# Kernel tuning notes

Measured on AMD Instinct MI355X. Metric: run time of the kernel, lower is better.

Reference implementation:

```python
import jax, jax.numpy as jnp
import numpy as np

T, B, I, H = 1200, 32, 512, 512


def setup_inputs() -> dict:
    key = jax.random.key(0)
    ks = jax.random.split(key, 10)
    s = 0.1
    x = jax.random.normal(ks[0], (T, B, I), dtype=jnp.float32)
    lengths = jax.random.randint(ks[1], (B,), 1, T + 1)
    lengths = lengths.at[0].set(T)  # ensure padded output length == T (static shape)
    return {
        "x": x,
        "output_lengths": lengths,
        "w_ih_fwd": jax.random.normal(ks[2], (4 * H, I), dtype=jnp.float32) * s,
        "w_hh_fwd": jax.random.normal(ks[3], (4 * H, H), dtype=jnp.float32) * s,
        "b_ih_fwd": jax.random.normal(ks[4], (4 * H,), dtype=jnp.float32) * s,
        "b_hh_fwd": jax.random.normal(ks[5], (4 * H,), dtype=jnp.float32) * s,
        "w_ih_bwd": jax.random.normal(ks[6], (4 * H, I), dtype=jnp.float32) * s,
        "w_hh_bwd": jax.random.normal(ks[7], (4 * H, H), dtype=jnp.float32) * s,
        "b_ih_bwd": jax.random.normal(ks[8], (4 * H,), dtype=jnp.float32) * s,
        "b_hh_bwd": jax.random.normal(ks[9], (4 * H,), dtype=jnp.float32) * s,
    }


def _lstm_dir(x, mask, w_ih, w_hh, b_ih, b_hh):
    """Masked unidirectional LSTM (PyTorch gate order i,f,g,o).
    x: (T,B,I), mask: (T,B,1) bool. Returns outputs (T,B,H), (h_n, c_n)."""
    h0 = jnp.zeros((x.shape[1], w_hh.shape[1]), dtype=x.dtype)
    c0 = jnp.zeros_like(h0)
    # Precompute input projection for all timesteps at once (one big GEMM).
    x_proj = jnp.einsum('tbi,gi->tbg', x, w_ih) + (b_ih + b_hh)

    def step(carry, inp):
        h, c = carry
        xp, m = inp  # xp: (B,4H), m: (B,1)
        gates = xp + h @ w_hh.T
        i, f, g, o = jnp.split(gates, 4, axis=-1)
        i = jax.nn.sigmoid(i)
        f = jax.nn.sigmoid(f)
        g = jnp.tanh(g)
        o = jax.nn.sigmoid(o)
        c_new = f * c + i * g
        h_new = o * jnp.tanh(c_new)
        # Packed semantics: state frozen past each sequence's length.
        h = jnp.where(m, h_new, h)
        c = jnp.where(m, c_new, c)
        out = jnp.where(m, h_new, jnp.zeros_like(h_new))  # pad positions -> 0
        return (h, c), out

    (h_n, c_n), outs = jax.lax.scan(step, (h0, c0), (x_proj, mask))
    return outs, h_n, c_n


def reference(x, output_lengths, w_ih_fwd, w_hh_fwd, b_ih_fwd, b_hh_fwd,
              w_ih_bwd, w_hh_bwd, b_ih_bwd, b_hh_bwd):
    t_idx = jnp.arange(x.shape[0])  # (T,)
    mask = (t_idx[:, None] < output_lengths[None, :])[:, :, None]  # (T,B,1)

    # Forward direction.
    out_f, h_f, c_f = _lstm_dir(x, mask, w_ih_fwd, w_hh_fwd, b_ih_fwd, b_hh_fwd)

    # Backward direction: reverse each sequence within its valid region.
    rev_idx = jnp.clip(output_lengths[None, :] - 1 - t_idx[:, None], 0)  # (T,B)
    x_rev = jnp.take_along_axis(x, rev_idx[:, :, None], axis=0) * mask
    out_r, h_b, c_b = _lstm_dir(x_rev, mask, w_ih_bwd, w_hh_bwd, b_ih_bwd, b_hh_bwd)
    out_b = jnp.take_along_axis(out_r, rev_idx[:, :, None], axis=0) * mask

    # Bidirectional view(...,2,-1).sum(2) == sum of direction outputs.
    out = out_f + out_b
    h_n = jnp.stack([h_f, h_b], axis=0)  # (2,B,H)
    c_n = jnp.stack([c_f, c_b], axis=0)
    return out, h_n, c_n
```

## Files before the change

kernel.cpp:

```cpp
#include <hip/hip_runtime.h>
#include <cstdint>
#include <cstddef>

typedef unsigned short u16;
typedef unsigned int u32;
typedef unsigned long long u64;
typedef short bf16x8 __attribute__((ext_vector_type(8)));
typedef float f32x4 __attribute__((ext_vector_type(4)));
typedef unsigned short u16x4 __attribute__((ext_vector_type(4)));

#define T_LEN 1200

#define O_X     0ull
#define O_WIH   39321600ull
#define O_WHH   43515904ull
#define O_BIAS  47710208ull
#define O_HBUF  47726592ull
#define WS_NEED 47988736ull

#define HO 19660800ull
#define CO 19693568ull

#define HROW 516

__device__ __forceinline__ u16 f2bf(float f) {
  union { float f; unsigned u; } v; v.f = f;
  unsigned r = v.u + 0x7FFFu + ((v.u >> 16) & 1u);
  return (u16)(r >> 16);
}
__device__ __forceinline__ float sigm(float x) { return 1.f / (1.f + __expf(-x)); }
__device__ __forceinline__ float tanh_s(float x) {
  float ax = fabsf(x);
  float e = __expf(-2.f * ax);
  float t = (1.f - e) / (1.f + e);
  return x < 0.f ? -t : t;
}

__device__ __forceinline__ u64 ld_dev64(const u32* p) {
  return __hip_atomic_load((const u64*)p, __ATOMIC_RELAXED, __HIP_MEMORY_SCOPE_AGENT);
}
__device__ __forceinline__ void st_dev32(u32* p, unsigned v) {
  __hip_atomic_store(p, v, __ATOMIC_RELAXED, __HIP_MEMORY_SCOPE_AGENT);
}

__global__ __launch_bounds__(256) void cast_x_k(const float4* __restrict__ x,
                                                u16* __restrict__ xb) {
  int i = blockIdx.x * 256 + threadIdx.x;
  float4 v = x[i];
  u16x4 o;
  o.x = f2bf(v.x); o.y = f2bf(v.y); o.z = f2bf(v.z); o.w = f2bf(v.w);
  *(u16x4*)(xb + (size_t)i * 4) = o;
}

__global__ __launch_bounds__(256) void prep_w_k(
    const float* __restrict__ wih_f, const float* __restrict__ whh_f,
    const float* __restrict__ bih_f, const float* __restrict__ bhh_f,
    const float* __restrict__ wih_b, const float* __restrict__ whh_b,
    const float* __restrict__ bih_b, const float* __restrict__ bhh_b,
    u16* __restrict__ Wih, u16* __restrict__ Whh, float* __restrict__ bias) {
  int tid = blockIdx.x * 256 + threadIdx.x;
  int g = tid >> 9;
  float vi, vh;
  if (g < 2048) { vi = wih_f[tid]; vh = whh_f[tid]; }
  else { int t2 = tid - (2048 * 512); vi = wih_b[t2]; vh = whh_b[t2]; }
  Wih[tid] = f2bf(vi);
  Whh[tid] = f2bf(vh);
  if ((tid & 511) == 0) {
    bias[g] = (g < 2048) ? (bih_f[g] + bhh_f[g]) : (bih_b[g - 2048] + bhh_b[g - 2048]);
  }
}

__global__ __launch_bounds__(256, 1) void lstm_rec(const u16* __restrict__ X,
                                                   const u16* __restrict__ Wih,
                                                   const u16* __restrict__ Whh,
                                                   const float* __restrict__ bias,
                                                   const int* __restrict__ lengths,
                                                   u32* __restrict__ hbuf,
                                                   float* __restrict__ out) {
  const int tid = threadIdx.x, lane = tid & 63, wid = tid >> 6;
  const int bx = blockIdx.x;
  const int dir = bx >> 5, slice = bx & 31, c0 = slice * 16;
  const int quad = lane >> 4, l15 = lane & 15;

  __shared__ alignas(16) u16 h_l[32 * HROW];
  __shared__ float pre[4][32][16];
  __shared__ int len_s[32];

  if (tid < 32) len_s[tid] = lengths[tid];

  bf16x8 bh[16], bxw[16];
  {
    const size_t wrow = (size_t)(dir * 2048 + wid * 512 + c0 + l15) * 512 + quad * 8;
#pragma unroll
    for (int ks = 0; ks < 16; ++ks) {
      bh[ks]  = *(const bf16x8*)(Whh + wrow + (size_t)ks * 32);
      bxw[ks] = *(const bf16x8*)(Wih + wrow + (size_t)ks * 32);
    }
  }
  __syncthreads();

  const int b0 = tid >> 4, colv = tid & 15, b1 = b0 + 16;
  const int hcol = c0 + colv;
  const float bi  = bias[dir * 2048 + 0 * 512 + hcol];
  const float bfv = bias[dir * 2048 + 1 * 512 + hcol];
  const float bg  = bias[dir * 2048 + 2 * 512 + hcol];
  const float bo  = bias[dir * 2048 + 3 * 512 + hcol];

  float hreg0 = 0.f, hreg1 = 0.f, creg0 = 0.f, creg1 = 0.f;
  const int len0 = len_s[b0], len1 = len_s[b1];
  const int lena = len_s[l15], lenb = len_s[16 + l15];

  for (int t = 0; t < T_LEN; ++t) {
    u32* cur = hbuf + (size_t)(((t & 1) * 2 + dir) * 16384);
    u32* nxt = hbuf + (size_t)((((t + 1) & 1) * 2 + dir) * 16384);

    int tta = (dir == 0) ? t : (lena - 1 - t);  if (tta < 0) tta = 0;
    int ttb = (dir == 0) ? t : (lenb - 1 - t);  if (ttb < 0) ttb = 0;
    const u16* xrow0 = X + ((size_t)tta * 32 + l15) * 512 + quad * 8;
    const u16* xrow1 = X + ((size_t)ttb * 32 + 16 + l15) * 512 + quad * 8;
    bf16x8 ax0[16], ax1[16];
#pragma unroll
    for (int ks = 0; ks < 16; ++ks) {
      ax0[ks] = *(const bf16x8*)(xrow0 + (size_t)ks * 32);
      ax1[ks] = *(const bf16x8*)(xrow1 + (size_t)ks * 32);
    }

    u64 stg[32];
#pragma unroll
    for (int j = 0; j < 32; ++j)
      stg[j] = ld_dev64(cur + j * 512 + tid * 2);

    f32x4 a0 = {0.f,0.f,0.f,0.f}, a1 = {0.f,0.f,0.f,0.f};
#pragma unroll
    for (int ks = 0; ks < 16; ++ks) {
      a0 = __builtin_amdgcn_mfma_f32_16x16x32_bf16(ax0[ks], bxw[ks], a0, 0, 0, 0);
      a1 = __builtin_amdgcn_mfma_f32_16x16x32_bf16(ax1[ks], bxw[ks], a1, 0, 0, 0);
    }

    const u64 e2 = ((u64)(u32)t << 32) | (u32)t;
    for (;;) {
      u64 bad = 0;
#pragma unroll
      for (int j = 0; j < 32; ++j) bad |= (stg[j] ^ e2);
      if ((bad & 0x0000FFFF0000FFFFull) == 0) break;
#pragma unroll
      for (int j = 0; j < 32; ++j)
        stg[j] = ld_dev64(cur + j * 512 + tid * 2);
    }

#pragma unroll
    for (int j = 0; j < 32; ++j) {
      u32 d0 = (u32)stg[j], d1 = (u32)(stg[j] >> 32);
      *(u32*)&h_l[j * HROW + tid * 2] = (d0 >> 16) | (d1 & 0xFFFF0000u);
    }
    __syncthreads();

    const u16* hl0 = h_l + (size_t)l15 * HROW + quad * 8;
    const u16* hl1 = h_l + (size_t)(16 + l15) * HROW + quad * 8;
#pragma unroll
    for (int ks = 0; ks < 16; ++ks) {
      bf16x8 f0 = *(const bf16x8*)(hl0 + ks * 32);
      bf16x8 f1 = *(const bf16x8*)(hl1 + ks * 32);
      a0 = __builtin_amdgcn_mfma_f32_16x16x32_bf16(f0, bh[ks], a0, 0, 0, 0);
      a1 = __builtin_amdgcn_mfma_f32_16x16x32_bf16(f1, bh[ks], a1, 0, 0, 0);
    }
#pragma unroll
    for (int r = 0; r < 4; ++r) {
      pre[wid][quad * 4 + r][l15]      = a0[r];
      pre[wid][16 + quad * 4 + r][l15] = a1[r];
    }
    __syncthreads();

    int tt0 = (dir == 0) ? t : (len0 - 1 - t);
    int tt1 = (dir == 0) ? t : (len1 - 1 - t);
    bool m0 = (dir == 0) ? (t < len0) : (tt0 >= 0);
    bool m1 = (dir == 0) ? (t < len1) : (tt1 >= 0);
    if (tt0 < 0) tt0 = 0;
    if (tt1 < 0) tt1 = 0;

    float hn0 = 0.f, hn1 = 0.f;
    if (m0) {
      float gi = pre[0][b0][colv] + bi,  gf = pre[1][b0][colv] + bfv;
      float gg = pre[2][b0][colv] + bg,  go = pre[3][b0][colv] + bo;
      float cn = sigm(gf) * creg0 + sigm(gi) * tanh_s(gg);
      hn0 = sigm(go) * tanh_s(cn);
      creg0 = cn; hreg0 = hn0;
    }
    if (m1) {
      float gi = pre[0][b1][colv] + bi,  gf = pre[1][b1][colv] + bfv;
      float gg = pre[2][b1][colv] + bg,  go = pre[3][b1][colv] + bo;
      float cn = sigm(gf) * creg1 + sigm(gi) * tanh_s(gg);
      hn1 = sigm(go) * tanh_s(cn);
      creg1 = cn; hreg1 = hn1;
    }

    const u32 tag = (u32)(t + 1);
    st_dev32(nxt + (size_t)b0 * 512 + hcol, ((u32)f2bf(hreg0) << 16) | tag);
    st_dev32(nxt + (size_t)b1 * 512 + hcol, ((u32)f2bf(hreg1) << 16) | tag);

    if (m0) atomicAdd(out + (size_t)(tt0 * 32 + b0) * 512 + hcol, hn0);
    if (m1) atomicAdd(out + (size_t)(tt1 * 32 + b1) * 512 + hcol, hn1);
  }

  out[HO + (size_t)dir * 16384 + (size_t)b0 * 512 + hcol] = hreg0;
  out[HO + (size_t)dir * 16384 + (size_t)b1 * 512 + hcol] = hreg1;
  out[CO + (size_t)dir * 16384 + (size_t)b0 * 512 + hcol] = creg0;
  out[CO + (size_t)dir * 16384 + (size_t)b1 * 512 + hcol] = creg1;
}

extern "C" void kernel_launch(void* const* d_in, const int* in_sizes, int n_in,
                              void* d_out, int out_size, void* d_ws, size_t ws_size,
                              hipStream_t stream) {
  const float* x     = (const float*)d_in[0];
  const int*   lens  = (const int*)d_in[1];
  const float* wih_f = (const float*)d_in[2];
  const float* whh_f = (const float*)d_in[3];
  const float* bih_f = (const float*)d_in[4];
  const float* bhh_f = (const float*)d_in[5];
  const float* wih_b = (const float*)d_in[6];
  const float* whh_b = (const float*)d_in[7];
  const float* bih_b = (const float*)d_in[8];
  const float* bhh_b = (const float*)d_in[9];
  float* out = (float*)d_out;
  char* ws = (char*)d_ws;

  u16*   xb   = (u16*)(ws + O_X);
  u16*   Wih  = (u16*)(ws + O_WIH);
  u16*   Whh  = (u16*)(ws + O_WHH);
  float* bias = (float*)(ws + O_BIAS);
  u32*   hbuf = (u32*)(ws + O_HBUF);

  hipMemsetAsync(hbuf, 0, 262144, stream);
  hipMemsetAsync(d_out, 0, (size_t)out_size * 4, stream);

  cast_x_k<<<19200, 256, 0, stream>>>((const float4*)x, xb);
  prep_w_k<<<8192, 256, 0, stream>>>(wih_f, whh_f, bih_f, bhh_f,
                                     wih_b, whh_b, bih_b, bhh_b, Wih, Whh, bias);
  lstm_rec<<<64, 256, 0, stream>>>(xb, Wih, Whh, bias, lens, hbuf, out);
}
```

Before: 11.26 ms.

## Co-locate each LSTM direction on one XCC and keep others busy spinning

The kernel now launches 256 blocks and uses the hardware XCC id to assign all 32 slices of a direction to the same XCC, so the per-step h exchange stays within one L2. It replaces the agent-scope atomic loads and stores with plain accesses plus an explicit cache invalidate on retry. Blocks on a third XCC run a dummy FMA spin loop, apparently to hold clocks up, and the rest exit. The x input tile is staged through LDS with split accumulators, and output atomicAdds are batched every 8 steps. This relies on undocumented XCC placement and on cache-coherence assumptions that may not hold for cross-XCC writes, and the spinning blocks burn power.

Measured after the change: 16.58 ms. +47.2%, slower.

```diff
diff --git a/kernel.cpp b/kernel.cpp
--- a/kernel.cpp
+++ b/kernel.cpp
@@ -16,7 +16,8 @@
 #define O_WHH   43515904ull
 #define O_BIAS  47710208ull
 #define O_HBUF  47726592ull
-#define WS_NEED 47988736ull
+#define O_CTL   47988736ull
+#define WS_NEED 47989248ull
 
 #define HO 19660800ull
 #define CO 19693568ull
@@ -34,13 +35,6 @@
   float e = __expf(-2.f * ax);
   float t = (1.f - e) / (1.f + e);
   return x < 0.f ? -t : t;
-}
-
-__device__ __forceinline__ u64 ld_dev64(const u32* p) {
-  return __hip_atomic_load((const u64*)p, __ATOMIC_RELAXED, __HIP_MEMORY_SCOPE_AGENT);
-}
-__device__ __forceinline__ void st_dev32(u32* p, unsigned v) {
-  __hip_atomic_store(p, v, __ATOMIC_RELAXED, __HIP_MEMORY_SCOPE_AGENT);
 }
 
 __global__ __launch_bounds__(256) void cast_x_k(const float4* __restrict__ x,
@@ -76,15 +70,70 @@
                                                    const float* __restrict__ bias,
                                                    const int* __restrict__ lengths,
                                                    u32* __restrict__ hbuf,
-                                                   float* __restrict__ out) {
+                                                   float* __restrict__ out,
+                                                   int* __restrict__ ctl) {
   const int tid = threadIdx.x, lane = tid & 63, wid = tid >> 6;
-  const int bx = blockIdx.x;
-  const int dir = bx >> 5, slice = bx & 31, c0 = slice * 16;
   const int quad = lane >> 4, l15 = lane & 15;
 
   __shared__ alignas(16) u16 h_l[32 * HROW];
+  __shared__ alignas(16) u16 x_l[32 * HROW];
   __shared__ float pre[4][32][16];
+  __shared__ float s_out[8 * 512];
   __shared__ int len_s[32];
+  __shared__ int s_dir, s_slice, s_done;
+
+  if (tid == 0) {
+    int xcc;
+    asm volatile("s_getreg_b32 %0, hwreg(HW_REG_XCC_ID)" : "=s"(xcc));
+    xcc &= 7;
+    int slot = __hip_atomic_fetch_add(&ctl[xcc], 1, __ATOMIC_RELAXED,
+                                      __HIP_MEMORY_SCOPE_AGENT);
+    int mydir;
+    if (slot == 0) {
+      int d = __hip_atomic_fetch_add(&ctl[16], 1, __ATOMIC_RELAXED,
+                                     __HIP_MEMORY_SCOPE_AGENT);
+      mydir = (d < 2) ? d : 2;
+      __hip_atomic_store(&ctl[8 + xcc], mydir + 1, __ATOMIC_RELAXED,
+                         __HIP_MEMORY_SCOPE_AGENT);
+    } else if (slot < 32) {
+      int v;
+      do {
+        v = __hip_atomic_load(&ctl[8 + xcc], __ATOMIC_RELAXED,
+                              __HIP_MEMORY_SCOPE_AGENT);
+        if (v == 0) __builtin_amdgcn_s_sleep(2);
+      } while (v == 0);
+      mydir = v - 1;
+    } else {
+      mydir = 3;
+    }
+    s_dir = mydir;
+    s_slice = (slot < 32) ? slot : 0;
+    s_done = 0;
+  }
+  __syncthreads();
+
+  if (s_dir == 3) return;
+  if (s_dir == 2) {
+    float a0 = tid * 0.5f + 1.f, a1 = tid * 0.25f + 2.f;
+    float a2 = tid * 0.125f + 3.f, a3 = tid * 0.0625f + 4.f;
+    for (;;) {
+#pragma unroll 64
+      for (int i = 0; i < 512; ++i) {
+        a0 = __builtin_fmaf(a0, 0.9999999f, 1e-9f);
+        a1 = __builtin_fmaf(a1, 0.9999998f, 2e-9f);
+        a2 = __builtin_fmaf(a2, 0.9999997f, 3e-9f);
+        a3 = __builtin_fmaf(a3, 0.9999996f, 4e-9f);
+      }
+      if (tid == 0)
+        *(volatile int*)&s_done = __hip_atomic_load(&ctl[17], __ATOMIC_RELAXED,
+                                                    __HIP_MEMORY_SCOPE_AGENT);
+      if (*(volatile int*)&s_done) break;
+    }
+    if (a0 + a1 + a2 + a3 == 3.14159f) out[0] = a0;
+    return;
+  }
+
+  const int dir = s_dir, slice = s_slice, c0 = slice * 16;
 
   if (tid < 32) len_s[tid] = lengths[tid];
 
@@ -108,34 +157,28 @@
 
   float hreg0 = 0.f, hreg1 = 0.f, creg0 = 0.f, creg1 = 0.f;
   const int len0 = len_s[b0], len1 = len_s[b1];
-  const int lena = len_s[l15], lenb = len_s[16 + l15];
+  const int xr = tid >> 3, seg = tid & 7;
+  const int lenxr = len_s[xr];
 
   for (int t = 0; t < T_LEN; ++t) {
     u32* cur = hbuf + (size_t)(((t & 1) * 2 + dir) * 16384);
     u32* nxt = hbuf + (size_t)((((t + 1) & 1) * 2 + dir) * 16384);
 
-    int tta = (dir == 0) ? t : (lena - 1 - t);  if (tta < 0) tta = 0;
-    int ttb = (dir == 0) ? t : (lenb - 1 - t);  if (ttb < 0) ttb = 0;
-    const u16* xrow0 = X + ((size_t)tta * 32 + l15) * 512 + quad * 8;
-    const u16* xrow1 = X + ((size_t)ttb * 32 + 16 + l15) * 512 + quad * 8;
-    bf16x8 ax0[16], ax1[16];
-#pragma unroll
-    for (int ks = 0; ks < 16; ++ks) {
-      ax0[ks] = *(const bf16x8*)(xrow0 + (size_t)ks * 32);
-      ax1[ks] = *(const bf16x8*)(xrow1 + (size_t)ks * 32);
-    }
+    int ttx = (dir == 0) ? t : (lenxr - 1 - t);  if (ttx < 0) ttx = 0;
+    const u16* xg = X + ((size_t)ttx * 32 + xr) * 512;
+    bf16x8 xv[8];
+#pragma unroll
+    for (int k = 0; k < 8; ++k)
+      xv[k] = *(const bf16x8*)(xg + k * 64 + seg * 8);
 
     u64 stg[32];
 #pragma unroll
     for (int j = 0; j < 32; ++j)
-      stg[j] = ld_dev64(cur + j * 512 + tid * 2);
-
-    f32x4 a0 = {0.f,0.f,0.f,0.f}, a1 = {0.f,0.f,0.f,0.f};
-#pragma unroll
-    for (int ks = 0; ks < 16; ++ks) {
-      a0 = __builtin_amdgcn_mfma_f32_16x16x32_bf16(ax0[ks], bxw[ks], a0, 0, 0, 0);
-      a1 = __builtin_amdgcn_mfma_f32_16x16x32_bf16(ax1[ks], bxw[ks], a1, 0, 0, 0);
-    }
+      stg[j] = *(const u64*)(cur + j * 512 + tid * 2);
+
+#pragma unroll
+    for (int k = 0; k < 8; ++k)
+      *(bf16x8*)&x_l[xr * HROW + k * 64 + seg * 8] = xv[k];
 
     const u64 e2 = ((u64)(u32)t << 32) | (u32)t;
     for (;;) {
@@ -143,9 +186,10 @@
 #pragma unroll
       for (int j = 0; j < 32; ++j) bad |= (stg[j] ^ e2);
       if ((bad & 0x0000FFFF0000FFFFull) == 0) break;
+      asm volatile("buffer_inv sc1" ::: "memory");
 #pragma unroll
       for (int j = 0; j < 32; ++j)
-        stg[j] = ld_dev64(cur + j * 512 + tid * 2);
+        stg[j] = *(const u64*)(cur + j * 512 + tid * 2);
     }
 
 #pragma unroll
@@ -155,38 +199,36 @@
     }
     __syncthreads();
 
+    f32x4 a0x = {0.f,0.f,0.f,0.f}, a1x = {0.f,0.f,0.f,0.f};
+    f32x4 a0h = {0.f,0.f,0.f,0.f}, a1h = {0.f,0.f,0.f,0.f};
+    const u16* xl0 = x_l + (size_t)l15 * HROW + quad * 8;
+    const u16* xl1 = x_l + (size_t)(16 + l15) * HROW + quad * 8;
     const u16* hl0 = h_l + (size_t)l15 * HROW + quad * 8;
     const u16* hl1 = h_l + (size_t)(16 + l15) * HROW + quad * 8;
 #pragma unroll
     for (int ks = 0; ks < 16; ++ks) {
-      bf16x8 f0 = *(const bf16x8*)(hl0 + ks * 32);
-      bf16x8 f1 = *(const bf16x8*)(hl1 + ks * 32);
-      a0 = __builtin_amdgcn_mfma_f32_16x16x32_bf16(f0, bh[ks], a0, 0, 0, 0);
-      a1 = __builtin_amdgcn_mfma_f32_16x16x32_bf16(f1, bh[ks], a1, 0, 0, 0);
-    }
+      a0x = __builtin_amdgcn_mfma_f32_16x16x32_bf16(*(const bf16x8*)(xl0 + ks * 32), bxw[ks], a0x, 0, 0, 0);
+      a1x = __builtin_amdgcn_mfma_f32_16x16x32_bf16(*(const bf16x8*)(xl1 + ks * 32), bxw[ks], a1x, 0, 0, 0);
+      a0h = __builtin_amdgcn_mfma_f32_16x16x32_bf16(*(const bf16x8*)(hl0 + ks * 32), bh[ks],  a0h, 0, 0, 0);
+      a1h = __builtin_amdgcn_mfma_f32_16x16x32_bf16(*(const bf16x8*)(hl1 + ks * 32), bh[ks],  a1h, 0, 0, 0);
+    }
+    f32x4 acc0 = a0x + a0h, acc1 = a1x + a1h;
 #pragma unroll
     for (int r = 0; r < 4; ++r) {
-      pre[wid][quad * 4 + r][l15]      = a0[r];
-      pre[wid][16 + quad * 4 + r][l15] = a1[r];
+      pre[wid][quad * 4 + r][l15]      = acc0[r];
+      pre[wid][16 + quad * 4 + r][l15] = acc1[r];
     }
     __syncthreads();
 
-    int tt0 = (dir == 0) ? t : (len0 - 1 - t);
-    int tt1 = (dir == 0) ? t : (len1 - 1 - t);
-    bool m0 = (dir == 0) ? (t < len0) : (tt0 >= 0);
-    bool m1 = (dir == 0) ? (t < len1) : (tt1 >= 0);
-    if (tt0 < 0) tt0 = 0;
-    if (tt1 < 0) tt1 = 0;
-
     float hn0 = 0.f, hn1 = 0.f;
-    if (m0) {
+    if (t < len0) {
       float gi = pre[0][b0][colv] + bi,  gf = pre[1][b0][colv] + bfv;
       float gg = pre[2][b0][colv] + bg,  go = pre[3][b0][colv] + bo;
       float cn = sigm(gf) * creg0 + sigm(gi) * tanh_s(gg);
       hn0 = sigm(go) * tanh_s(cn);
       creg0 = cn; hreg0 = hn0;
     }
-    if (m1) {
+    if (t < len1) {
       float gi = pre[0][b1][colv] + bi,  gf = pre[1][b1][colv] + bfv;
       float gg = pre[2][b1][colv] + bg,  go = pre[3][b1][colv] + bo;
       float cn = sigm(gf) * creg1 + sigm(gi) * tanh_s(gg);
@@ -195,17 +237,35 @@
     }
 
     const u32 tag = (u32)(t + 1);
-    st_dev32(nxt + (size_t)b0 * 512 + hcol, ((u32)f2bf(hreg0) << 16) | tag);
-    st_dev32(nxt + (size_t)b1 * 512 + hcol, ((u32)f2bf(hreg1) << 16) | tag);
-
-    if (m0) atomicAdd(out + (size_t)(tt0 * 32 + b0) * 512 + hcol, hn0);
-    if (m1) atomicAdd(out + (size_t)(tt1 * 32 + b1) * 512 + hcol, hn1);
+    nxt[(size_t)b0 * 512 + hcol] = ((u32)f2bf(hreg0) << 16) | tag;
+    nxt[(size_t)b1 * 512 + hcol] = ((u32)f2bf(hreg1) << 16) | tag;
+    asm volatile("" ::: "memory");
+
+    s_out[(t & 7) * 512 + tid]       = hn0;
+    s_out[(t & 7) * 512 + 256 + tid] = hn1;
+    if ((t & 7) == 7) {
+#pragma unroll
+      for (int k = 0; k < 8; ++k) {
+        int ts = t - 7 + k;
+        if (ts < len0) {
+          int tt = (dir == 0) ? ts : (len0 - 1 - ts);
+          atomicAdd(out + (size_t)(tt * 32 + b0) * 512 + hcol, s_out[k * 512 + tid]);
+        }
+        if (ts < len1) {
+          int tt = (dir == 0) ? ts : (len1 - 1 - ts);
+          atomicAdd(out + (size_t)(tt * 32 + b1) * 512 + hcol, s_out[k * 512 + 256 + tid]);
+        }
+      }
+    }
   }
 
   out[HO + (size_t)dir * 16384 + (size_t)b0 * 512 + hcol] = hreg0;
   out[HO + (size_t)dir * 16384 + (size_t)b1 * 512 + hcol] = hreg1;
   out[CO + (size_t)dir * 16384 + (size_t)b0 * 512 + hcol] = creg0;
   out[CO + (size_t)dir * 16384 + (size_t)b1 * 512 + hcol] = creg1;
+
+  if (tid == 0)
+    __hip_atomic_store(&ctl[17], 1, __ATOMIC_RELAXED, __HIP_MEMORY_SCOPE_AGENT);
 }
 
 extern "C" void kernel_launch(void* const* d_in, const int* in_sizes, int n_in,
@@ -229,12 +289,13 @@
   u16*   Whh  = (u16*)(ws + O_WHH);
   float* bias = (float*)(ws + O_BIAS);
   u32*   hbuf = (u32*)(ws + O_HBUF);
-
-  hipMemsetAsync(hbuf, 0, 262144, stream);
+  int*   ctl  = (int*)(ws + O_CTL);
+
+  hipMemsetAsync(hbuf, 0, 262144 + 512, stream);
   hipMemsetAsync(d_out, 0, (size_t)out_size * 4, stream);
 
   cast_x_k<<<19200, 256, 0, stream>>>((const float4*)x, xb);
   prep_w_k<<<8192, 256, 0, stream>>>(wih_f, whh_f, bih_f, bhh_f,
                                      wih_b, whh_b, bih_b, bhh_b, Wih, Whh, bias);
-  lstm_rec<<<64, 256, 0, stream>>>(xb, Wih, Whh, bias, lens, hbuf, out);
-}
+  lstm_rec<<<256, 256, 0, stream>>>(xb, Wih, Whh, bias, lens, hbuf, out, ctl);
+}
```

## Prefetch next-step x fragments and batch output atomics every eight steps

Applied to the files above, without the earlier changes.

The x-projection operands for step t+1 are loaded right after the spin-wait on the hidden-state buffer, so their global latency overlaps the h-exchange and recurrent MFMAs rather than sitting on the critical path at the start of each step. Separate accumulators for the input and recurrent MFMAs let the input projection issue independently before being summed. Output atomics are buffered in shared memory and flushed every eight steps, taking the per-step global atomics off the loop body. This costs extra registers for the prefetched fragments and 16KB of LDS, and since T is a multiple of eight every buffered step is flushed.

Result: faster. 11.02 ms (-2.2%).

```diff
diff --git a/kernel.cpp b/kernel.cpp
--- a/kernel.cpp
+++ b/kernel.cpp
@@ -84,6 +84,7 @@
 
   __shared__ alignas(16) u16 h_l[32 * HROW];
   __shared__ float pre[4][32][16];
+  __shared__ float s_out[8 * 512];
   __shared__ int len_s[32];
 
   if (tid < 32) len_s[tid] = lengths[tid];
@@ -108,33 +109,36 @@
 
   float hreg0 = 0.f, hreg1 = 0.f, creg0 = 0.f, creg1 = 0.f;
   const int len0 = len_s[b0], len1 = len_s[b1];
-  const int lena = len_s[l15], lenb = len_s[16 + l15];
+  const int ba = l15, bb = 16 + l15;
+  const int lena = len_s[ba], lenb = len_s[bb];
+
+  bf16x8 ax0[16], ax1[16];
+  {
+    int tta = (dir == 0) ? 0 : (lena - 1);  if (tta < 0) tta = 0;
+    int ttb = (dir == 0) ? 0 : (lenb - 1);  if (ttb < 0) ttb = 0;
+    const u16* xrow0 = X + ((size_t)tta * 32 + ba) * 512 + quad * 8;
+    const u16* xrow1 = X + ((size_t)ttb * 32 + bb) * 512 + quad * 8;
+#pragma unroll
+    for (int ks = 0; ks < 16; ++ks) {
+      ax0[ks] = *(const bf16x8*)(xrow0 + (size_t)ks * 32);
+      ax1[ks] = *(const bf16x8*)(xrow1 + (size_t)ks * 32);
+    }
+  }
 
   for (int t = 0; t < T_LEN; ++t) {
     u32* cur = hbuf + (size_t)(((t & 1) * 2 + dir) * 16384);
     u32* nxt = hbuf + (size_t)((((t + 1) & 1) * 2 + dir) * 16384);
 
-    int tta = (dir == 0) ? t : (lena - 1 - t);  if (tta < 0) tta = 0;
-    int ttb = (dir == 0) ? t : (lenb - 1 - t);  if (ttb < 0) ttb = 0;
-    const u16* xrow0 = X + ((size_t)tta * 32 + l15) * 512 + quad * 8;
-    const u16* xrow1 = X + ((size_t)ttb * 32 + 16 + l15) * 512 + quad * 8;
-    bf16x8 ax0[16], ax1[16];
-#pragma unroll
-    for (int ks = 0; ks < 16; ++ks) {
-      ax0[ks] = *(const bf16x8*)(xrow0 + (size_t)ks * 32);
-      ax1[ks] = *(const bf16x8*)(xrow1 + (size_t)ks * 32);
-    }
-
     u64 stg[32];
 #pragma unroll
     for (int j = 0; j < 32; ++j)
       stg[j] = ld_dev64(cur + j * 512 + tid * 2);
 
-    f32x4 a0 = {0.f,0.f,0.f,0.f}, a1 = {0.f,0.f,0.f,0.f};
-#pragma unroll
-    for (int ks = 0; ks < 16; ++ks) {
-      a0 = __builtin_amdgcn_mfma_f32_16x16x32_bf16(ax0[ks], bxw[ks], a0, 0, 0, 0);
-      a1 = __builtin_amdgcn_mfma_f32_16x16x32_bf16(ax1[ks], bxw[ks], a1, 0, 0, 0);
+    f32x4 a0x = {0.f,0.f,0.f,0.f}, a1x = {0.f,0.f,0.f,0.f};
+#pragma unroll
+    for (int ks = 0; ks < 16; ++ks) {
+      a0x = __builtin_amdgcn_mfma_f32_16x16x32_bf16(ax0[ks], bxw[ks], a0x, 0, 0, 0);
+      a1x = __builtin_amdgcn_mfma_f32_16x16x32_bf16(ax1[ks], bxw[ks], a1x, 0, 0, 0);
     }
 
     const u64 e2 = ((u64)(u32)t << 32) | (u32)t;
@@ -148,6 +152,21 @@
         stg[j] = ld_dev64(cur + j * 512 + tid * 2);
     }
 
+    {
+      int tn = t + 1;
+      int tta = (dir == 0) ? (tn < T_LEN ? tn : T_LEN - 1) : (lena - 1 - tn);
+      int ttb = (dir == 0) ? (tn < T_LEN ? tn : T_LEN - 1) : (lenb - 1 - tn);
+      if (tta < 0) tta = 0;
+      if (ttb < 0) ttb = 0;
+      const u16* xrow0 = X + ((size_t)tta * 32 + ba) * 512 + quad * 8;
+      const u16* xrow1 = X + ((size_t)ttb * 32 + bb) * 512 + quad * 8;
+#pragma unroll
+      for (int ks = 0; ks < 16; ++ks) {
+        ax0[ks] = *(const bf16x8*)(xrow0 + (size_t)ks * 32);
+        ax1[ks] = *(const bf16x8*)(xrow1 + (size_t)ks * 32);
+      }
+    }
+
 #pragma unroll
     for (int j = 0; j < 32; ++j) {
       u32 d0 = (u32)stg[j], d1 = (u32)(stg[j] >> 32);
@@ -155,38 +174,33 @@
     }
     __syncthreads();
 
+    f32x4 a0h = {0.f,0.f,0.f,0.f}, a1h = {0.f,0.f,0.f,0.f};
     const u16* hl0 = h_l + (size_t)l15 * HROW + quad * 8;
     const u16* hl1 = h_l + (size_t)(16 + l15) * HROW + quad * 8;
 #pragma unroll
     for (int ks = 0; ks < 16; ++ks) {
       bf16x8 f0 = *(const bf16x8*)(hl0 + ks * 32);
       bf16x8 f1 = *(const bf16x8*)(hl1 + ks * 32);
-      a0 = __builtin_amdgcn_mfma_f32_16x16x32_bf16(f0, bh[ks], a0, 0, 0, 0);
-      a1 = __builtin_amdgcn_mfma_f32_16x16x32_bf16(f1, bh[ks], a1, 0, 0, 0);
-    }
+      a0h = __builtin_amdgcn_mfma_f32_16x16x32_bf16(f0, bh[ks], a0h, 0, 0, 0);
+      a1h = __builtin_amdgcn_mfma_f32_16x16x32_bf16(f1, bh[ks], a1h, 0, 0, 0);
+    }
+    f32x4 acc0 = a0x + a0h, acc1 = a1x + a1h;
 #pragma unroll
     for (int r = 0; r < 4; ++r) {
-      pre[wid][quad * 4 + r][l15]      = a0[r];
-      pre[wid][16 + quad * 4 + r][l15] = a1[r];
+      pre[wid][quad * 4 + r][l15]      = acc0[r];
+      pre[wid][16 + quad * 4 + r][l15] = acc1[r];
     }
     __syncthreads();
 
-    int tt0 = (dir == 0) ? t : (len0 - 1 - t);
-    int tt1 = (dir == 0) ? t : (len1 - 1 - t);
-    bool m0 = (dir == 0) ? (t < len0) : (tt0 >= 0);
-    bool m1 = (dir == 0) ? (t < len1) : (tt1 >= 0);
-    if (tt0 < 0) tt0 = 0;
-    if (tt1 < 0) tt1 = 0;
-
     float hn0 = 0.f, hn1 = 0.f;
-    if (m0) {
+    if (t < len0) {
       float gi = pre[0][b0][colv] + bi,  gf = pre[1][b0][colv] + bfv;
       float gg = pre[2][b0][colv] + bg,  go = pre[3][b0][colv] + bo;
       float cn = sigm(gf) * creg0 + sigm(gi) * tanh_s(gg);
       hn0 = sigm(go) * tanh_s(cn);
       creg0 = cn; hreg0 = hn0;
     }
-    if (m1) {
+    if (t < len1) {
       float gi = pre[0][b1][colv] + bi,  gf = pre[1][b1][colv] + bfv;
       float gg = pre[2][b1][colv] + bg,  go = pre[3][b1][colv] + bo;
       float cn = sigm(gf) * creg1 + sigm(gi) * tanh_s(gg);
@@ -198,8 +212,22 @@
     st_dev32(nxt + (size_t)b0 * 512 + hcol, ((u32)f2bf(hreg0) << 16) | tag);
     st_dev32(nxt + (size_t)b1 * 512 + hcol, ((u32)f2bf(hreg1) << 16) | tag);
 
-    if (m0) atomicAdd(out + (size_t)(tt0 * 32 + b0) * 512 + hcol, hn0);
-    if (m1) atomicAdd(out + (size_t)(tt1 * 32 + b1) * 512 + hcol, hn1);
+    s_out[(t & 7) * 512 + tid]       = hn0;
+    s_out[(t & 7) * 512 + 256 + tid] = hn1;
+    if ((t & 7) == 7) {
+#pragma unroll
+      for (int k = 0; k < 8; ++k) {
+        int ts = t - 7 + k;
+        if (ts < len0) {
+          int tt = (dir == 0) ? ts : (len0 - 1 - ts);
+          atomicAdd(out + (size_t)(tt * 32 + b0) * 512 + hcol, s_out[k * 512 + tid]);
+        }
+        if (ts < len1) {
+          int tt = (dir == 0) ? ts : (len1 - 1 - ts);
+          atomicAdd(out + (size_t)(tt * 32 + b1) * 512 + hcol, s_out[k * 512 + 256 + tid]);
+        }
+      }
+    }
   }
 
   out[HO + (size_t)dir * 16384 + (size_t)b0 * 512 + hcol] = hreg0;
```
